# Kernel optimization log

Hardware: AMD Instinct MI355X
Metric: run time of the kernel (lower is better)

## Reference

```python
import jax, jax.numpy as jnp
import numpy as np

B = 65536
E = 1024      # embedding_dim
NC = 8        # num_chunks
CD = E // NC  # chunk_dim = 128
H = 2         # num_heads
QK = 32       # qk_dim
VD = 64       # v_dim
LN_EPS = 1e-5


def _sinusoidal_pe():
    pos = np.arange(NC, dtype=np.float32)[:, None]
    div = np.exp(np.arange(0, CD, 2, dtype=np.float32) * (-np.log(10000.0) / CD))
    pe = np.zeros((NC, CD), dtype=np.float32)
    pe[:, 0::2] = np.sin(pos * div)
    pe[:, 1::2] = np.cos(pos * div)
    return jnp.asarray(pe)


def _rel_index():
    c = np.arange(NC)
    return jnp.asarray(c[None, :] - c[:, None] + (NC - 1))  # [NC, NC] in [0, 2*NC-2]


def setup_inputs() -> dict:
    key = jax.random.key(0)
    ks = jax.random.split(key, 6)
    x = jax.random.normal(ks[0], (B, E), dtype=jnp.float32)
    Wq = jax.random.normal(ks[1], (H * QK, CD), dtype=jnp.float32) * 0.02
    Wk = jax.random.normal(ks[2], (H * QK, CD), dtype=jnp.float32) * 0.02
    Wv = jax.random.normal(ks[3], (H * VD, CD), dtype=jnp.float32) * 0.02
    Wo = jax.random.normal(ks[4], (CD, H * VD), dtype=jnp.float32) * 0.02
    gamma = jnp.ones((CD,), dtype=jnp.float32)
    beta = jnp.zeros((CD,), dtype=jnp.float32)
    # relative_pos_bias init: bias[:, i] = -0.5 * |i - (NC-1)|
    dist = np.abs(np.arange(2 * NC - 1) - (NC - 1)).astype(np.float32)
    rel_bias = jnp.broadcast_to(jnp.asarray(-0.5 * dist), (H, 2 * NC - 1)).copy()
    return {"x": x, "Wq": Wq, "Wk": Wk, "Wv": Wv, "Wo": Wo,
            "gamma": gamma, "beta": beta, "rel_bias": rel_bias}


def reference(x, Wq, Wk, Wv, Wo, gamma, beta, rel_bias):
    pe = _sinusoidal_pe()           # [NC, CD]
    idx = _rel_index()              # [NC, NC] int
    scale = QK ** -0.5

    xc = x.reshape(-1, NC, CD) + pe[None]                     # [B, NC, CD]
    Q = (xc @ Wq.T).reshape(-1, NC, H, QK).transpose(0, 2, 1, 3)  # [B,H,NC,QK]
    K = (xc @ Wk.T).reshape(-1, NC, H, QK).transpose(0, 2, 1, 3)
    V = (xc @ Wv.T).reshape(-1, NC, H, VD).transpose(0, 2, 1, 3)  # [B,H,NC,VD]

    scores = jnp.einsum('bhnq,bhmq->bhnm', Q, K) * scale          # [B,H,NC,NC]
    scores = scores + rel_bias[:, idx][None]                      # gathered rel-pos bias
    attn = jax.nn.softmax(scores, axis=-1)                        # dropout = identity (eval)

    ctx = jnp.einsum('bhnm,bhmv->bhnv', attn, V)                  # [B,H,NC,VD]
    ctx = ctx.transpose(0, 2, 1, 3).reshape(-1, NC, H * VD)       # [B,NC,H*VD]
    out = ctx @ Wo.T                                              # [B,NC,CD]

    h = xc + out
    mu = jnp.mean(h, axis=-1, keepdims=True)
    var = jnp.var(h, axis=-1, keepdims=True)
    y = (h - mu) * jax.lax.rsqrt(var + LN_EPS) * gamma + beta
    return y.reshape(-1, E), attn
```

## Files before the change

### kernel.cpp

```cpp
#include <hip/hip_runtime.h>

typedef __attribute__((ext_vector_type(8))) short bf16x8;
typedef __attribute__((ext_vector_type(4))) float f32x4;
typedef __attribute__((ext_vector_type(2))) unsigned int u32x2;

__device__ __forceinline__ unsigned short f2bf(float f) {
  union { float f; unsigned u; } a; a.f = f;
  return (unsigned short)((a.u + 0x7fffu + ((a.u >> 16) & 1u)) >> 16);
}
__device__ __forceinline__ unsigned pk2bf(float lo, float hi) {
  return (unsigned)f2bf(lo) | ((unsigned)f2bf(hi) << 16);
}

union UB8 { bf16x8 v; unsigned d[4]; };

__global__ void wconv_kernel(const float* __restrict__ Wq, const float* __restrict__ Wk,
                             const float* __restrict__ Wv, const float* __restrict__ Wo,
                             unsigned short* __restrict__ ws) {
  int i = blockIdx.x * 256 + threadIdx.x;
  float v;
  if (i < 8192) v = Wq[i];
  else if (i < 16384) v = Wk[i - 8192];
  else if (i < 32768) v = Wv[i - 16384];
  else v = Wo[i - 32768];
  ws[i] = f2bf(v);
}

__global__ __launch_bounds__(256, 3)
void wlmha_kernel(const float* __restrict__ x,
                  const unsigned short* __restrict__ wA,
                  const unsigned short* __restrict__ wOb,
                  const float* __restrict__ gamma,
                  const float* __restrict__ beta,
                  const float* __restrict__ relb,
                  float* __restrict__ y_out,
                  float* __restrict__ attn_out)
{
  const int t = threadIdx.x;
  const int l = t & 63;
  const int w = t >> 6;
  const long b0 = (long)blockIdx.x * 8;

  __shared__ __align__(16) char smem[49280];
  float* peS  = (float*)smem;
  char*  qkS  = smem;
  char*  vtS  = smem + 16384;
  char*  hbS  = smem;
  char*  xcS  = smem + 32768;
  float* s_rel = (float*)(smem + 49152);

  f32x4 xr[4][2];
  {
    const float* xb = x + b0 * 1024;
#pragma unroll
    for (int i = 0; i < 4; ++i) {
      const float* p = xb + (t + 256 * i) * 8;
      xr[i][0] = *(const f32x4*)p;
      xr[i][1] = *(const f32x4*)(p + 4);
    }
  }
  bf16x8 wf[4][4];
#pragma unroll
  for (int nb = 0; nb < 4; ++nb) {
    const unsigned short* src = wA + (w * 64 + nb * 16 + (l & 15)) * 128 + (l >> 4) * 8;
#pragma unroll
    for (int ks = 0; ks < 4; ++ks) wf[nb][ks] = *(const bf16x8*)(src + ks * 32);
  }
  for (int e = t; e < 512; e += 256) {
    const int c = e >> 6, i = e & 63;
    const float div = expf(-0.14391156831212727f * (float)i);
    float s, co;
    sincosf((float)c * div, &s, &co);
    peS[c * 132 + 2 * i]     = s;
    peS[c * 132 + 2 * i + 1] = co;
  }
  if (t < 30) s_rel[(t / 15) * 16 + (t % 15)] = relb[t];
  __syncthreads();

#pragma unroll
  for (int i = 0; i < 4; ++i) {
    const int g = t + 256 * i;
    const int m = g >> 4;
    const int c = (g & 15) * 8;
    const float* per = peS + (m & 7) * 132 + c;
    UB8 fr;
#pragma unroll
    for (int j = 0; j < 4; ++j) { xr[i][0][j] += per[j]; xr[i][1][j] += per[4 + j]; }
    fr.d[0] = pk2bf(xr[i][0][0], xr[i][0][1]);
    fr.d[1] = pk2bf(xr[i][0][2], xr[i][0][3]);
    fr.d[2] = pk2bf(xr[i][1][0], xr[i][1][1]);
    fr.d[3] = pk2bf(xr[i][1][2], xr[i][1][3]);
    *(bf16x8*)(xcS + m * 256 + ((c * 2) ^ ((m & 7) << 4))) = fr.v;
  }
  __syncthreads();

#pragma unroll
  for (int mt = 0; mt < 4; ++mt) {
    bf16x8 xf[4];
    const int row = mt * 16 + (l & 15);
#pragma unroll
    for (int ks = 0; ks < 4; ++ks)
      xf[ks] = *(const bf16x8*)(xcS + row * 256 + ((ks * 64 + (l >> 4) * 16) ^ ((row & 7) << 4)));
    if (w < 2) {
#pragma unroll
      for (int nb = 0; nb < 4; ++nb) {
        f32x4 acc = {0.f, 0.f, 0.f, 0.f};
#pragma unroll
        for (int ks = 0; ks < 4; ++ks)
          acc = __builtin_amdgcn_mfma_f32_16x16x32_bf16(wf[nb][ks], xf[ks], acc, 0, 0, 0);
        u32x2 pk; pk.x = pk2bf(acc[0], acc[1]); pk.y = pk2bf(acc[2], acc[3]);
        const int colb = (w * 128 + nb * 32 + (l >> 4) * 8) ^ ((row & 7) << 4);
        *(u32x2*)(qkS + row * 256 + colb) = pk;
      }
    } else {
#pragma unroll
      for (int nb = 0; nb < 4; ++nb) {
        f32x4 acc = {0.f, 0.f, 0.f, 0.f};
#pragma unroll
        for (int ks = 0; ks < 4; ++ks)
          acc = __builtin_amdgcn_mfma_f32_16x16x32_bf16(xf[ks], wf[nb][ks], acc, 0, 0, 0);
        const int nv = (w - 2) * 64 + nb * 16 + (l & 15);
        const int rb = mt * 16 + (l >> 4) * 4;
        u32x2 pk; pk.x = pk2bf(acc[0], acc[1]); pk.y = pk2bf(acc[2], acc[3]);
        *(u32x2*)(vtS + nv * 128 + ((rb * 2) ^ ((nv & 7) << 4))) = pk;
      }
    }
  }
  __syncthreads();

  bf16x8 wof[2][4];
#pragma unroll
  for (int nt = 0; nt < 2; ++nt) {
    const unsigned short* src = wOb + (w * 32 + nt * 16 + (l & 15)) * 128 + (l >> 4) * 8;
#pragma unroll
    for (int ks = 0; ks < 4; ++ks) wof[nt][ks] = *(const bf16x8*)(src + ks * 32);
  }
  {
    const int h  = w >> 1;
    const int qc = l & 7;
    const int g4 = l >> 4;
    const bool valid = ((l >> 5) & 1) == ((l >> 3) & 1);
    float bias[4];
#pragma unroll
    for (int j = 0; j < 4; ++j)
      bias[j] = s_rel[h * 16 + (g4 & 1) * 4 + j - qc + 7];

#pragma unroll
    for (int uu = 0; uu < 2; ++uu) {
      const int T = (w & 1) * 2 + uu;
      const int row = T * 16 + (l & 15);
      const int sw = (row & 7) << 4;
      bf16x8 kf = *(const bf16x8*)(qkS + row * 256 + ((128 + h * 64 + g4 * 16) ^ sw));
      bf16x8 qf = *(const bf16x8*)(qkS + row * 256 + ((h * 64 + g4 * 16) ^ sw));
      f32x4 zero = {0.f, 0.f, 0.f, 0.f};
      f32x4 st = __builtin_amdgcn_mfma_f32_16x16x32_bf16(kf, qf, zero, 0, 0, 0);
      float s0[4];
#pragma unroll
      for (int j = 0; j < 4; ++j)
        s0[j] = valid ? st[j] * 0.17677669529663687f + bias[j] : -1e30f;
      float mx = fmaxf(fmaxf(s0[0], s0[1]), fmaxf(s0[2], s0[3]));
      mx = fmaxf(mx, __shfl_xor(mx, 16));
      mx = fmaxf(mx, __shfl_xor(mx, 32));
      float p[4], sum = 0.f;
#pragma unroll
      for (int j = 0; j < 4; ++j) { p[j] = __expf(s0[j] - mx); sum += p[j]; }
      sum += __shfl_xor(sum, 16);
      sum += __shfl_xor(sum, 32);
      const float inv = 1.0f / sum;
#pragma unroll
      for (int j = 0; j < 4; ++j) p[j] *= inv;

      if (valid) {
        float* ap = attn_out + ((b0 + (row >> 3)) * 2 + h) * 64 + qc * 8 + (g4 & 1) * 4;
        f32x4 pv = {p[0], p[1], p[2], p[3]};
        *(f32x4*)ap = pv;
      }

      const unsigned P0 = pk2bf(p[0], p[1]);
      const unsigned P1 = pk2bf(p[2], p[3]);
      const int sA = (l & 15) + (g4 & 1) * 32;
      UB8 pf;
      pf.d[0] = (unsigned)__shfl((int)P0, sA);
      pf.d[1] = (unsigned)__shfl((int)P1, sA);
      pf.d[2] = (unsigned)__shfl((int)P0, sA + 16);
      pf.d[3] = (unsigned)__shfl((int)P1, sA + 16);
      if (g4 >= 2) { pf.d[0] = 0; pf.d[1] = 0; pf.d[2] = 0; pf.d[3] = 0; }

#pragma unroll
      for (int vb = 0; vb < 4; ++vb) {
        const int nv = h * 64 + vb * 16 + (l & 15);
        const int kb = (32 * T + 16 * (g4 & 1)) ^ ((nv & 7) << 4);
        bf16x8 vf = *(const bf16x8*)(vtS + nv * 128 + kb);
        f32x4 c = __builtin_amdgcn_mfma_f32_16x16x32_bf16(vf, pf.v, zero, 0, 0, 0);
        u32x2 pk; pk.x = pk2bf(c[0], c[1]); pk.y = pk2bf(c[2], c[3]);
        const int fb = (h * 128 + vb * 32 + g4 * 8) ^ sw;
        *(u32x2*)(xcS + row * 256 + fb) = pk;
      }
    }
  }
  __syncthreads();

  const int cg = (t & 15) * 8;
  f32x4 gm0 = *(const f32x4*)(gamma + cg);
  f32x4 gm1 = *(const f32x4*)(gamma + cg + 4);
  f32x4 bt0 = *(const f32x4*)(beta + cg);
  f32x4 bt1 = *(const f32x4*)(beta + cg + 4);

#pragma unroll
  for (int mt = 0; mt < 4; ++mt) {
    bf16x8 cf[4];
    const int row = mt * 16 + (l & 15);
#pragma unroll
    for (int ks = 0; ks < 4; ++ks)
      cf[ks] = *(const bf16x8*)(xcS + row * 256 + ((ks * 64 + (l >> 4) * 16) ^ ((row & 7) << 4)));
#pragma unroll
    for (int nt = 0; nt < 2; ++nt) {
      f32x4 acc = {0.f, 0.f, 0.f, 0.f};
#pragma unroll
      for (int ks = 0; ks < 4; ++ks)
        acc = __builtin_amdgcn_mfma_f32_16x16x32_bf16(wof[nt][ks], cf[ks], acc, 0, 0, 0);
      const int colb = ((w * 32 + nt * 16 + (l >> 4) * 4) * 4) ^ ((row & 7) << 4);
      *(f32x4*)(hbS + row * 512 + colb) = acc;
    }
  }
  __syncthreads();

  {
    float* yb = y_out + b0 * 1024;
#pragma unroll
    for (int i = 0; i < 4; ++i) {
      const int g = t + 256 * i;
      const int m = g >> 4;
      const int sw = (m & 7) << 4;
      const char* hp = hbS + m * 512;
      f32x4 h0 = *(const f32x4*)(hp + ((cg * 4) ^ sw));
      f32x4 h1 = *(const f32x4*)(hp + ((cg * 4 + 16) ^ sw));
      float sum = 0.f, sq = 0.f;
#pragma unroll
      for (int j = 0; j < 4; ++j) {
        h0[j] += xr[i][0][j]; h1[j] += xr[i][1][j];
        sum += h0[j] + h1[j];
        sq  += h0[j] * h0[j] + h1[j] * h1[j];
      }
#pragma unroll
      for (int d = 1; d < 16; d <<= 1) {
        sum += __shfl_xor(sum, d);
        sq  += __shfl_xor(sq, d);
      }
      const float mu = sum * 0.0078125f;
      const float rs = rsqrtf(sq * 0.0078125f - mu * mu + 1e-5f);
      f32x4 o0, o1;
#pragma unroll
      for (int j = 0; j < 4; ++j) {
        o0[j] = (h0[j] - mu) * rs * gm0[j] + bt0[j];
        o1[j] = (h1[j] - mu) * rs * gm1[j] + bt1[j];
      }
      *(f32x4*)(yb + g * 8) = o0;
      *(f32x4*)(yb + g * 8 + 4) = o1;
    }
  }
}

extern "C" void kernel_launch(void* const* d_in, const int* in_sizes, int n_in,
                              void* d_out, int out_size, void* d_ws, size_t ws_size,
                              hipStream_t stream) {
  (void)in_sizes; (void)n_in; (void)out_size; (void)ws_size;
  const float* x    = (const float*)d_in[0];
  const float* Wq   = (const float*)d_in[1];
  const float* Wk   = (const float*)d_in[2];
  const float* Wv   = (const float*)d_in[3];
  const float* Wo   = (const float*)d_in[4];
  const float* gam  = (const float*)d_in[5];
  const float* bet  = (const float*)d_in[6];
  const float* relb = (const float*)d_in[7];
  float* y    = (float*)d_out;
  float* attn = y + (size_t)65536 * 1024;
  unsigned short* ws = (unsigned short*)d_ws;

  hipLaunchKernelGGL(wconv_kernel, dim3(192), dim3(256), 0, stream, Wq, Wk, Wv, Wo, ws);
  hipLaunchKernelGGL(wlmha_kernel, dim3(8192), dim3(256), 0, stream,
                     x, ws, ws + 32768, gam, bet, relb, y, attn);
}
```

Baseline: 172.2 us.

## Make blocks persistent over four batch groups and prefetch next x tile

```diff
diff --git a/kernel.cpp b/kernel.cpp
--- a/kernel.cpp
+++ b/kernel.cpp
@@ -4,259 +4,293 @@
 typedef __attribute__((ext_vector_type(4))) float f32x4;
 typedef __attribute__((ext_vector_type(2))) unsigned int u32x2;
 
+union UB8 { bf16x8 v; unsigned d[4]; unsigned short u[8]; };
+
+__device__ __forceinline__ float bf2f(unsigned short u) {
+  union { unsigned u; float f; } a; a.u = ((unsigned)u) << 16;
+  return a.f;
+}
+__device__ __forceinline__ unsigned pk2bf(float lo, float hi) {
+  union { __bf16 b[2]; unsigned u; } r;
+  r.b[0] = (__bf16)lo; r.b[1] = (__bf16)hi;
+  return r.u;
+}
 __device__ __forceinline__ unsigned short f2bf(float f) {
   union { float f; unsigned u; } a; a.f = f;
   return (unsigned short)((a.u + 0x7fffu + ((a.u >> 16) & 1u)) >> 16);
 }
-__device__ __forceinline__ unsigned pk2bf(float lo, float hi) {
-  return (unsigned)f2bf(lo) | ((unsigned)f2bf(hi) << 16);
-}
-
-union UB8 { bf16x8 v; unsigned d[4]; };
-
-__global__ void wconv_kernel(const float* __restrict__ Wq, const float* __restrict__ Wk,
-                             const float* __restrict__ Wv, const float* __restrict__ Wo,
-                             unsigned short* __restrict__ ws) {
-  int i = blockIdx.x * 256 + threadIdx.x;
-  float v;
-  if (i < 8192) v = Wq[i];
-  else if (i < 16384) v = Wk[i - 8192];
-  else if (i < 32768) v = Wv[i - 16384];
-  else v = Wo[i - 32768];
-  ws[i] = f2bf(v);
-}
+
+__global__ void prep_kernel(const float* __restrict__ Wq, const float* __restrict__ Wk,
+                            const float* __restrict__ Wv, const float* __restrict__ Wo,
+                            unsigned short* __restrict__ ws) {
+  const int b = blockIdx.x;
+  if (b < 192) {
+    int i = b * 256 + threadIdx.x;
+    float v;
+    if (i < 8192) v = Wq[i];
+    else if (i < 16384) v = Wk[i - 8192];
+    else if (i < 32768) v = Wv[i - 16384];
+    else v = Wo[i - 32768];
+    ws[i] = f2bf(v);
+  } else {
+    float* pe = (float*)(ws + 49152);
+#pragma unroll
+    for (int k = 0; k < 4; ++k) {
+      int e = threadIdx.x * 4 + k;
+      int c = e >> 7, col = e & 127;
+      float div = expf(-0.14391156831212727f * (float)(col >> 1));
+      float ang = (float)c * div;
+      pe[e] = (col & 1) ? cosf(ang) : sinf(ang);
+    }
+  }
+}
+
+#define NG 4
 
 __global__ __launch_bounds__(256, 3)
 void wlmha_kernel(const float* __restrict__ x,
                   const unsigned short* __restrict__ wA,
                   const unsigned short* __restrict__ wOb,
+                  const float* __restrict__ peG,
                   const float* __restrict__ gamma,
                   const float* __restrict__ beta,
                   const float* __restrict__ relb,
                   float* __restrict__ y_out,
                   float* __restrict__ attn_out)
 {
-  const int t = threadIdx.x;
-  const int l = t & 63;
-  const int w = t >> 6;
-  const long b0 = (long)blockIdx.x * 8;
+  const int t   = threadIdx.x;
+  const int l   = t & 63;
+  const int w   = t >> 6;
+  const int mr0 = t >> 4;
+  const int cg  = (t & 15) * 8;
+  const int sw0 = (mr0 & 7) << 4;
 
   __shared__ __align__(16) char smem[49280];
-  float* peS  = (float*)smem;
-  char*  qkS  = smem;
-  char*  vtS  = smem + 16384;
-  char*  hbS  = smem;
-  char*  xcS  = smem + 32768;
+  char* qkS = smem;
+  char* vtS = smem + 16384;
+  char* hbS = smem;
+  char* xcS = smem + 32768;
   float* s_rel = (float*)(smem + 49152);
 
-  f32x4 xr[4][2];
+  const long g0 = (long)blockIdx.x * NG;
+  f32x4 xg[4][2];
   {
-    const float* xb = x + b0 * 1024;
+    const float* xb = x + g0 * 8192;
 #pragma unroll
     for (int i = 0; i < 4; ++i) {
       const float* p = xb + (t + 256 * i) * 8;
-      xr[i][0] = *(const f32x4*)p;
-      xr[i][1] = *(const f32x4*)(p + 4);
+      xg[i][0] = *(const f32x4*)p;
+      xg[i][1] = *(const f32x4*)(p + 4);
     }
   }
-  bf16x8 wf[4][4];
-#pragma unroll
-  for (int nb = 0; nb < 4; ++nb) {
-    const unsigned short* src = wA + (w * 64 + nb * 16 + (l & 15)) * 128 + (l >> 4) * 8;
-#pragma unroll
-    for (int ks = 0; ks < 4; ++ks) wf[nb][ks] = *(const bf16x8*)(src + ks * 32);
-  }
-  for (int e = t; e < 512; e += 256) {
-    const int c = e >> 6, i = e & 63;
-    const float div = expf(-0.14391156831212727f * (float)i);
-    float s, co;
-    sincosf((float)c * div, &s, &co);
-    peS[c * 132 + 2 * i]     = s;
-    peS[c * 132 + 2 * i + 1] = co;
-  }
+  const f32x4 pe0 = *(const f32x4*)(peG + (mr0 & 7) * 128 + cg);
+  const f32x4 pe1 = *(const f32x4*)(peG + (mr0 & 7) * 128 + cg + 4);
   if (t < 30) s_rel[(t / 15) * 16 + (t % 15)] = relb[t];
-  __syncthreads();
-
-#pragma unroll
-  for (int i = 0; i < 4; ++i) {
-    const int g = t + 256 * i;
-    const int m = g >> 4;
-    const int c = (g & 15) * 8;
-    const float* per = peS + (m & 7) * 132 + c;
-    UB8 fr;
-#pragma unroll
-    for (int j = 0; j < 4; ++j) { xr[i][0][j] += per[j]; xr[i][1][j] += per[4 + j]; }
-    fr.d[0] = pk2bf(xr[i][0][0], xr[i][0][1]);
-    fr.d[1] = pk2bf(xr[i][0][2], xr[i][0][3]);
-    fr.d[2] = pk2bf(xr[i][1][0], xr[i][1][1]);
-    fr.d[3] = pk2bf(xr[i][1][2], xr[i][1][3]);
-    *(bf16x8*)(xcS + m * 256 + ((c * 2) ^ ((m & 7) << 4))) = fr.v;
-  }
-  __syncthreads();
-
-#pragma unroll
-  for (int mt = 0; mt < 4; ++mt) {
-    bf16x8 xf[4];
-    const int row = mt * 16 + (l & 15);
-#pragma unroll
-    for (int ks = 0; ks < 4; ++ks)
-      xf[ks] = *(const bf16x8*)(xcS + row * 256 + ((ks * 64 + (l >> 4) * 16) ^ ((row & 7) << 4)));
-    if (w < 2) {
-#pragma unroll
-      for (int nb = 0; nb < 4; ++nb) {
+
+  for (int ig = 0; ig < NG; ++ig) {
+    const long b0 = (g0 + ig) * 8;
+
+    bf16x8 wf[4][4];
+#pragma unroll
+    for (int nb = 0; nb < 4; ++nb) {
+      const unsigned short* src = wA + (w * 64 + nb * 16 + (l & 15)) * 128 + (l >> 4) * 8;
+#pragma unroll
+      for (int ks = 0; ks < 4; ++ks) wf[nb][ks] = *(const bf16x8*)(src + ks * 32);
+    }
+
+#pragma unroll
+    for (int i = 0; i < 4; ++i) {
+      const int m = mr0 + 16 * i;
+      f32x4 a0 = xg[i][0] + pe0;
+      f32x4 a1 = xg[i][1] + pe1;
+      UB8 fr;
+      fr.d[0] = pk2bf(a0[0], a0[1]);
+      fr.d[1] = pk2bf(a0[2], a0[3]);
+      fr.d[2] = pk2bf(a1[0], a1[1]);
+      fr.d[3] = pk2bf(a1[2], a1[3]);
+      *(bf16x8*)(xcS + m * 256 + ((cg * 2) ^ sw0)) = fr.v;
+    }
+    __syncthreads();
+
+    if (ig + 1 < NG) {
+      const float* xn = x + (g0 + ig + 1) * 8192;
+#pragma unroll
+      for (int i = 0; i < 4; ++i) {
+        const float* p = xn + (t + 256 * i) * 8;
+        xg[i][0] = *(const f32x4*)p;
+        xg[i][1] = *(const f32x4*)(p + 4);
+      }
+    }
+
+#pragma unroll
+    for (int mt = 0; mt < 4; ++mt) {
+      bf16x8 xf[4];
+      const int row = mt * 16 + (l & 15);
+#pragma unroll
+      for (int ks = 0; ks < 4; ++ks)
+        xf[ks] = *(const bf16x8*)(xcS + row * 256 + ((ks * 64 + (l >> 4) * 16) ^ ((row & 7) << 4)));
+      if (w < 2) {
+#pragma unroll
+        for (int nb = 0; nb < 4; ++nb) {
+          f32x4 acc = {0.f, 0.f, 0.f, 0.f};
+#pragma unroll
+          for (int ks = 0; ks < 4; ++ks)
+            acc = __builtin_amdgcn_mfma_f32_16x16x32_bf16(wf[nb][ks], xf[ks], acc, 0, 0, 0);
+          u32x2 pk; pk.x = pk2bf(acc[0], acc[1]); pk.y = pk2bf(acc[2], acc[3]);
+          const int colb = (w * 128 + nb * 32 + (l >> 4) * 8) ^ ((row & 7) << 4);
+          *(u32x2*)(qkS + row * 256 + colb) = pk;
+        }
+      } else {
+#pragma unroll
+        for (int nb = 0; nb < 4; ++nb) {
+          f32x4 acc = {0.f, 0.f, 0.f, 0.f};
+#pragma unroll
+          for (int ks = 0; ks < 4; ++ks)
+            acc = __builtin_amdgcn_mfma_f32_16x16x32_bf16(xf[ks], wf[nb][ks], acc, 0, 0, 0);
+          const int nv = (w - 2) * 64 + nb * 16 + (l & 15);
+          const int rb = mt * 16 + (l >> 4) * 4;
+          u32x2 pk; pk.x = pk2bf(acc[0], acc[1]); pk.y = pk2bf(acc[2], acc[3]);
+          *(u32x2*)(vtS + nv * 128 + ((rb * 2) ^ ((nv & 7) << 4))) = pk;
+        }
+      }
+    }
+    bf16x8 xcr[4];
+#pragma unroll
+    for (int i = 0; i < 4; ++i) {
+      const int m = mr0 + 16 * i;
+      xcr[i] = *(const bf16x8*)(xcS + m * 256 + ((cg * 2) ^ sw0));
+    }
+    __syncthreads();
+
+    bf16x8 wof[2][4];
+#pragma unroll
+    for (int nt = 0; nt < 2; ++nt) {
+      const unsigned short* src = wOb + (w * 32 + nt * 16 + (l & 15)) * 128 + (l >> 4) * 8;
+#pragma unroll
+      for (int ks = 0; ks < 4; ++ks) wof[nt][ks] = *(const bf16x8*)(src + ks * 32);
+    }
+    {
+      const int h  = w >> 1;
+      const int qc = l & 7;
+      const int g4 = l >> 4;
+      const bool valid = ((l >> 5) & 1) == ((l >> 3) & 1);
+      float bias[4];
+#pragma unroll
+      for (int j = 0; j < 4; ++j)
+        bias[j] = s_rel[h * 16 + (g4 & 1) * 4 + j - qc + 7];
+
+#pragma unroll
+      for (int uu = 0; uu < 2; ++uu) {
+        const int T = (w & 1) * 2 + uu;
+        const int row = T * 16 + (l & 15);
+        const int sw = (row & 7) << 4;
+        bf16x8 kf = *(const bf16x8*)(qkS + row * 256 + ((128 + h * 64 + g4 * 16) ^ sw));
+        bf16x8 qf = *(const bf16x8*)(qkS + row * 256 + ((h * 64 + g4 * 16) ^ sw));
+        f32x4 zero = {0.f, 0.f, 0.f, 0.f};
+        f32x4 st = __builtin_amdgcn_mfma_f32_16x16x32_bf16(kf, qf, zero, 0, 0, 0);
+        float s0[4];
+#pragma unroll
+        for (int j = 0; j < 4; ++j)
+          s0[j] = valid ? st[j] * 0.17677669529663687f + bias[j] : -1e30f;
+        float mx = fmaxf(fmaxf(s0[0], s0[1]), fmaxf(s0[2], s0[3]));
+        mx = fmaxf(mx, __shfl_xor(mx, 16));
+        mx = fmaxf(mx, __shfl_xor(mx, 32));
+        float p[4], sum = 0.f;
+#pragma unroll
+        for (int j = 0; j < 4; ++j) { p[j] = __expf(s0[j] - mx); sum += p[j]; }
+        sum += __shfl_xor(sum, 16);
+        sum += __shfl_xor(sum, 32);
+        const float inv = 1.0f / sum;
+#pragma unroll
+        for (int j = 0; j < 4; ++j) p[j] *= inv;
+
+        if (valid) {
+          float* ap = attn_out + ((b0 + (row >> 3)) * 2 + h) * 64 + qc * 8 + (g4 & 1) * 4;
+          f32x4 pv = {p[0], p[1], p[2], p[3]};
+          *(f32x4*)ap = pv;
+        }
+
+        const unsigned P0 = pk2bf(p[0], p[1]);
+        const unsigned P1 = pk2bf(p[2], p[3]);
+        const int sA = (l & 15) + (g4 & 1) * 32;
+        UB8 pf;
+        pf.d[0] = (unsigned)__shfl((int)P0, sA);
+        pf.d[1] = (unsigned)__shfl((int)P1, sA);
+        pf.d[2] = (unsigned)__shfl((int)P0, sA + 16);
+        pf.d[3] = (unsigned)__shfl((int)P1, sA + 16);
+        if (g4 >= 2) { pf.d[0] = 0; pf.d[1] = 0; pf.d[2] = 0; pf.d[3] = 0; }
+
+#pragma unroll
+        for (int vb = 0; vb < 4; ++vb) {
+          const int nv = h * 64 + vb * 16 + (l & 15);
+          const int kb = (32 * T + 16 * (g4 & 1)) ^ ((nv & 7) << 4);
+          bf16x8 vf = *(const bf16x8*)(vtS + nv * 128 + kb);
+          f32x4 c = __builtin_amdgcn_mfma_f32_16x16x32_bf16(vf, pf.v, zero, 0, 0, 0);
+          u32x2 pk; pk.x = pk2bf(c[0], c[1]); pk.y = pk2bf(c[2], c[3]);
+          const int fb = (h * 128 + vb * 32 + g4 * 8) ^ sw;
+          *(u32x2*)(xcS + row * 256 + fb) = pk;
+        }
+      }
+    }
+    __syncthreads();
+
+    const f32x4 gm0 = *(const f32x4*)(gamma + cg);
+    const f32x4 gm1 = *(const f32x4*)(gamma + cg + 4);
+    const f32x4 bt0 = *(const f32x4*)(beta + cg);
+    const f32x4 bt1 = *(const f32x4*)(beta + cg + 4);
+#pragma unroll
+    for (int mt = 0; mt < 4; ++mt) {
+      bf16x8 cf[4];
+      const int row = mt * 16 + (l & 15);
+#pragma unroll
+      for (int ks = 0; ks < 4; ++ks)
+        cf[ks] = *(const bf16x8*)(xcS + row * 256 + ((ks * 64 + (l >> 4) * 16) ^ ((row & 7) << 4)));
+#pragma unroll
+      for (int nt = 0; nt < 2; ++nt) {
         f32x4 acc = {0.f, 0.f, 0.f, 0.f};
 #pragma unroll
         for (int ks = 0; ks < 4; ++ks)
-          acc = __builtin_amdgcn_mfma_f32_16x16x32_bf16(wf[nb][ks], xf[ks], acc, 0, 0, 0);
-        u32x2 pk; pk.x = pk2bf(acc[0], acc[1]); pk.y = pk2bf(acc[2], acc[3]);
-        const int colb = (w * 128 + nb * 32 + (l >> 4) * 8) ^ ((row & 7) << 4);
-        *(u32x2*)(qkS + row * 256 + colb) = pk;
-      }
-    } else {
-#pragma unroll
-      for (int nb = 0; nb < 4; ++nb) {
-        f32x4 acc = {0.f, 0.f, 0.f, 0.f};
-#pragma unroll
-        for (int ks = 0; ks < 4; ++ks)
-          acc = __builtin_amdgcn_mfma_f32_16x16x32_bf16(xf[ks], wf[nb][ks], acc, 0, 0, 0);
-        const int nv = (w - 2) * 64 + nb * 16 + (l & 15);
-        const int rb = mt * 16 + (l >> 4) * 4;
-        u32x2 pk; pk.x = pk2bf(acc[0], acc[1]); pk.y = pk2bf(acc[2], acc[3]);
-        *(u32x2*)(vtS + nv * 128 + ((rb * 2) ^ ((nv & 7) << 4))) = pk;
-      }
-    }
-  }
-  __syncthreads();
-
-  bf16x8 wof[2][4];
-#pragma unroll
-  for (int nt = 0; nt < 2; ++nt) {
-    const unsigned short* src = wOb + (w * 32 + nt * 16 + (l & 15)) * 128 + (l >> 4) * 8;
-#pragma unroll
-    for (int ks = 0; ks < 4; ++ks) wof[nt][ks] = *(const bf16x8*)(src + ks * 32);
-  }
-  {
-    const int h  = w >> 1;
-    const int qc = l & 7;
-    const int g4 = l >> 4;
-    const bool valid = ((l >> 5) & 1) == ((l >> 3) & 1);
-    float bias[4];
-#pragma unroll
-    for (int j = 0; j < 4; ++j)
-      bias[j] = s_rel[h * 16 + (g4 & 1) * 4 + j - qc + 7];
-
-#pragma unroll
-    for (int uu = 0; uu < 2; ++uu) {
-      const int T = (w & 1) * 2 + uu;
-      const int row = T * 16 + (l & 15);
-      const int sw = (row & 7) << 4;
-      bf16x8 kf = *(const bf16x8*)(qkS + row * 256 + ((128 + h * 64 + g4 * 16) ^ sw));
-      bf16x8 qf = *(const bf16x8*)(qkS + row * 256 + ((h * 64 + g4 * 16) ^ sw));
-      f32x4 zero = {0.f, 0.f, 0.f, 0.f};
-      f32x4 st = __builtin_amdgcn_mfma_f32_16x16x32_bf16(kf, qf, zero, 0, 0, 0);
-      float s0[4];
-#pragma unroll
-      for (int j = 0; j < 4; ++j)
-        s0[j] = valid ? st[j] * 0.17677669529663687f + bias[j] : -1e30f;
-      float mx = fmaxf(fmaxf(s0[0], s0[1]), fmaxf(s0[2], s0[3]));
-      mx = fmaxf(mx, __shfl_xor(mx, 16));
-      mx = fmaxf(mx, __shfl_xor(mx, 32));
-      float p[4], sum = 0.f;
-#pragma unroll
-      for (int j = 0; j < 4; ++j) { p[j] = __expf(s0[j] - mx); sum += p[j]; }
-      sum += __shfl_xor(sum, 16);
-      sum += __shfl_xor(sum, 32);
-      const float inv = 1.0f / sum;
-#pragma unroll
-      for (int j = 0; j < 4; ++j) p[j] *= inv;
-
-      if (valid) {
-        float* ap = attn_out + ((b0 + (row >> 3)) * 2 + h) * 64 + qc * 8 + (g4 & 1) * 4;
-        f32x4 pv = {p[0], p[1], p[2], p[3]};
-        *(f32x4*)ap = pv;
-      }
-
-      const unsigned P0 = pk2bf(p[0], p[1]);
-      const unsigned P1 = pk2bf(p[2], p[3]);
-      const int sA = (l & 15) + (g4 & 1) * 32;
-      UB8 pf;
-      pf.d[0] = (unsigned)__shfl((int)P0, sA);
-      pf.d[1] = (unsigned)__shfl((int)P1, sA);
-      pf.d[2] = (unsigned)__shfl((int)P0, sA + 16);
-      pf.d[3] = (unsigned)__shfl((int)P1, sA + 16);
-      if (g4 >= 2) { pf.d[0] = 0; pf.d[1] = 0; pf.d[2] = 0; pf.d[3] = 0; }
-
-#pragma unroll
-      for (int vb = 0; vb < 4; ++vb) {
-        const int nv = h * 64 + vb * 16 + (l & 15);
-        const int kb = (32 * T + 16 * (g4 & 1)) ^ ((nv & 7) << 4);
-        bf16x8 vf = *(const bf16x8*)(vtS + nv * 128 + kb);
-        f32x4 c = __builtin_amdgcn_mfma_f32_16x16x32_bf16(vf, pf.v, zero, 0, 0, 0);
-        u32x2 pk; pk.x = pk2bf(c[0], c[1]); pk.y = pk2bf(c[2], c[3]);
-        const int fb = (h * 128 + vb * 32 + g4 * 8) ^ sw;
-        *(u32x2*)(xcS + row * 256 + fb) = pk;
-      }
-    }
-  }
-  __syncthreads();
-
-  const int cg = (t & 15) * 8;
-  f32x4 gm0 = *(const f32x4*)(gamma + cg);
-  f32x4 gm1 = *(const f32x4*)(gamma + cg + 4);
-  f32x4 bt0 = *(const f32x4*)(beta + cg);
-  f32x4 bt1 = *(const f32x4*)(beta + cg + 4);
-
-#pragma unroll
-  for (int mt = 0; mt < 4; ++mt) {
-    bf16x8 cf[4];
-    const int row = mt * 16 + (l & 15);
-#pragma unroll
-    for (int ks = 0; ks < 4; ++ks)
-      cf[ks] = *(const bf16x8*)(xcS + row * 256 + ((ks * 64 + (l >> 4) * 16) ^ ((row & 7) << 4)));
-#pragma unroll
-    for (int nt = 0; nt < 2; ++nt) {
-      f32x4 acc = {0.f, 0.f, 0.f, 0.f};
-#pragma unroll
-      for (int ks = 0; ks < 4; ++ks)
-        acc = __builtin_amdgcn_mfma_f32_16x16x32_bf16(wof[nt][ks], cf[ks], acc, 0, 0, 0);
-      const int colb = ((w * 32 + nt * 16 + (l >> 4) * 4) * 4) ^ ((row & 7) << 4);
-      *(f32x4*)(hbS + row * 512 + colb) = acc;
-    }
-  }
-  __syncthreads();
-
-  {
-    float* yb = y_out + b0 * 1024;
-#pragma unroll
-    for (int i = 0; i < 4; ++i) {
-      const int g = t + 256 * i;
-      const int m = g >> 4;
-      const int sw = (m & 7) << 4;
-      const char* hp = hbS + m * 512;
-      f32x4 h0 = *(const f32x4*)(hp + ((cg * 4) ^ sw));
-      f32x4 h1 = *(const f32x4*)(hp + ((cg * 4 + 16) ^ sw));
-      float sum = 0.f, sq = 0.f;
-#pragma unroll
-      for (int j = 0; j < 4; ++j) {
-        h0[j] += xr[i][0][j]; h1[j] += xr[i][1][j];
-        sum += h0[j] + h1[j];
-        sq  += h0[j] * h0[j] + h1[j] * h1[j];
-      }
-#pragma unroll
-      for (int d = 1; d < 16; d <<= 1) {
-        sum += __shfl_xor(sum, d);
-        sq  += __shfl_xor(sq, d);
-      }
-      const float mu = sum * 0.0078125f;
-      const float rs = rsqrtf(sq * 0.0078125f - mu * mu + 1e-5f);
-      f32x4 o0, o1;
-#pragma unroll
-      for (int j = 0; j < 4; ++j) {
-        o0[j] = (h0[j] - mu) * rs * gm0[j] + bt0[j];
-        o1[j] = (h1[j] - mu) * rs * gm1[j] + bt1[j];
-      }
-      *(f32x4*)(yb + g * 8) = o0;
-      *(f32x4*)(yb + g * 8 + 4) = o1;
+          acc = __builtin_amdgcn_mfma_f32_16x16x32_bf16(wof[nt][ks], cf[ks], acc, 0, 0, 0);
+        const int colb = ((w * 32 + nt * 16 + (l >> 4) * 4) * 4) ^ ((row & 7) << 4);
+        *(f32x4*)(hbS + row * 512 + colb) = acc;
+      }
+    }
+    __syncthreads();
+
+    {
+      float* yb = y_out + b0 * 1024;
+#pragma unroll
+      for (int i = 0; i < 4; ++i) {
+        const int m = mr0 + 16 * i;
+        const char* hp = hbS + m * 512;
+        f32x4 h0 = *(const f32x4*)(hp + ((cg * 4) ^ sw0));
+        f32x4 h1 = *(const f32x4*)(hp + ((cg * 4 + 16) ^ sw0));
+        UB8 r; r.v = xcr[i];
+        float sum = 0.f, sq = 0.f;
+#pragma unroll
+        for (int j = 0; j < 4; ++j) {
+          h0[j] += bf2f(r.u[j]);
+          h1[j] += bf2f(r.u[4 + j]);
+          sum += h0[j] + h1[j];
+          sq  += h0[j] * h0[j] + h1[j] * h1[j];
+        }
+#pragma unroll
+        for (int d = 1; d < 16; d <<= 1) {
+          sum += __shfl_xor(sum, d);
+          sq  += __shfl_xor(sq, d);
+        }
+        const float mu = sum * 0.0078125f;
+        const float rs = rsqrtf(sq * 0.0078125f - mu * mu + 1e-5f);
+        f32x4 o0, o1;
+#pragma unroll
+        for (int j = 0; j < 4; ++j) {
+          o0[j] = (h0[j] - mu) * rs * gm0[j] + bt0[j];
+          o1[j] = (h1[j] - mu) * rs * gm1[j] + bt1[j];
+        }
+        const int g = t + 256 * i;
+        *(f32x4*)(yb + g * 8) = o0;
+        *(f32x4*)(yb + g * 8 + 4) = o1;
+      }
     }
   }
 }
@@ -276,8 +310,9 @@
   float* y    = (float*)d_out;
   float* attn = y + (size_t)65536 * 1024;
   unsigned short* ws = (unsigned short*)d_ws;
-
-  hipLaunchKernelGGL(wconv_kernel, dim3(192), dim3(256), 0, stream, Wq, Wk, Wv, Wo, ws);
-  hipLaunchKernelGGL(wlmha_kernel, dim3(8192), dim3(256), 0, stream,
-                     x, ws, ws + 32768, gam, bet, relb, y, attn);
-}
+  const float* peG = (const float*)(ws + 49152);
+
+  hipLaunchKernelGGL(prep_kernel, dim3(193), dim3(256), 0, stream, Wq, Wk, Wv, Wo, ws);
+  hipLaunchKernelGGL(wlmha_kernel, dim3(2048), dim3(256), 0, stream,
+                     x, ws, ws + 32768, peG, gam, bet, relb, y, attn);
+}
```

Result: slower. 438.5 us (+154.7%).
